# Performance work log

Measured on AMD Instinct MI355X. Metric: run time of the kernel, lower is better.

The kernel has to match this reference:

```python
import jax, jax.numpy as jnp
import numpy as np

B, T, F = 2, 128, 88          # batch, time frames, pitch bins (hard-coded 88)
HIDDEN = 64                    # LSTM input dim
N_UNIT = 64                    # channel dim (= 2 * lstm hidden 32)
N_HEAD = 4
HEAD_DIM = N_UNIT // N_HEAD    # 16
WINDOW = 7
N_LAYERS = 2
DIFF_STEPS = 100
LSTM_H = N_UNIT // 2           # 32 per direction


def setup_inputs() -> dict:
    key = jax.random.key(0)
    ks = jax.random.split(key, 12)
    s = 0.05
    inp = {
        'x': jax.random.normal(ks[0], (B, T * F, HIDDEN), jnp.float32),
        't': jax.random.randint(ks[1], (B,), 0, DIFF_STEPS, jnp.int32),
        # LSTM params, stacked [layer, direction, ...]; layer-1 input dim == 2*LSTM_H == HIDDEN
        'lstm_w_ih': s * jax.random.normal(ks[2], (N_LAYERS, 2, 4 * LSTM_H, HIDDEN), jnp.float32),
        'lstm_w_hh': s * jax.random.normal(ks[3], (N_LAYERS, 2, 4 * LSTM_H, LSTM_H), jnp.float32),
        'lstm_b_ih': s * jax.random.normal(ks[4], (N_LAYERS, 2, 4 * LSTM_H), jnp.float32),
        'lstm_b_hh': s * jax.random.normal(ks[5], (N_LAYERS, 2, 4 * LSTM_H), jnp.float32),
        # per-NA-layer params
        't_emb': s * jax.random.normal(ks[6], (N_LAYERS, DIFF_STEPS, N_UNIT), jnp.float32),
        'w_qkv': s * jax.random.normal(ks[7], (N_LAYERS, N_UNIT, 3 * N_UNIT), jnp.float32),
        'b_qkv': jnp.zeros((N_LAYERS, 3 * N_UNIT), jnp.float32),
        'rpb': s * jax.random.normal(ks[8], (N_LAYERS, N_HEAD, 2 * WINDOW - 1, 2 * WINDOW - 1), jnp.float32),
        'w_proj': s * jax.random.normal(ks[9], (N_LAYERS, N_UNIT, N_UNIT), jnp.float32),
        'b_proj': jnp.zeros((N_LAYERS, N_UNIT), jnp.float32),
    }
    return inp


def _lstm_dir(x, w_ih, w_hh, b_ih, b_hh, reverse):
    # x: [N, T, D]; pytorch gate order i, f, g, o
    N = x.shape[0]
    H = w_hh.shape[1]
    xs = jnp.swapaxes(x, 0, 1)
    if reverse:
        xs = xs[::-1]
    b = b_ih + b_hh
    def step(carry, xt):
        h, c = carry
        g = xt @ w_ih.T + h @ w_hh.T + b
        i, f, gg, o = jnp.split(g, 4, axis=-1)
        c = jax.nn.sigmoid(f) * c + jax.nn.sigmoid(i) * jnp.tanh(gg)
        h = jax.nn.sigmoid(o) * jnp.tanh(c)
        return (h, c), h
    h0 = jnp.zeros((N, H), x.dtype)
    _, hs = jax.lax.scan(step, (h0, h0), xs)
    if reverse:
        hs = hs[::-1]
    return jnp.swapaxes(hs, 0, 1)


def _bilstm(x, w_ih, w_hh, b_ih, b_hh):
    for l in range(w_ih.shape[0]):
        fwd = _lstm_dir(x, w_ih[l, 0], w_hh[l, 0], b_ih[l, 0], b_hh[l, 0], False)
        bwd = _lstm_dir(x, w_ih[l, 1], w_hh[l, 1], b_ih[l, 1], b_hh[l, 1], True)
        x = jnp.concatenate([fwd, bwd], axis=-1)
    return x


def _nbh(L, w):
    # NATTEN-style clamped (non-shrinking) neighborhood window per axis
    i = jnp.arange(L)
    start = jnp.clip(i - w // 2, 0, L - w)
    idx = start[:, None] + jnp.arange(w)[None, :]   # [L, w] absolute neighbor idx
    rel = idx - i[:, None] + (w - 1)                # [L, w] rel-pos-bias idx in [0, 2w-2]
    return idx, rel


def _na2d(x, t_idx, emb, wqkv, bqkv, rpb_l, wproj, bproj):
    # x: [B, Th, Tw, C]; diffusion-step conditioning via learned embedding add
    Bx, Th, Tw, C = x.shape
    h = x + emb[t_idx][:, None, None, :]
    qkv = (h @ wqkv + bqkv).reshape(Bx, Th, Tw, 3, N_HEAD, HEAD_DIM)
    q = jnp.moveaxis(qkv[..., 0, :, :], 3, 1) * (HEAD_DIM ** -0.5)  # [B,h,Th,Tw,d]
    k = jnp.moveaxis(qkv[..., 1, :, :], 3, 1)
    v = jnp.moveaxis(qkv[..., 2, :, :], 3, 1)
    ih, rh = _nbh(Th, WINDOW)
    iw, rw = _nbh(Tw, WINDOW)
    # gather windowed neighbors: [B,h,Th,Tw,w,w,d]
    kn = k[:, :, ih[:, None, :, None], iw[None, :, None, :], :]
    vn = v[:, :, ih[:, None, :, None], iw[None, :, None, :], :]
    bias = rpb_l[:, rh[:, None, :, None], rw[None, :, None, :]]     # [h,Th,Tw,w,w]
    logits = jnp.einsum('bhijd,bhijkld->bhijkl', q, kn) + bias[None]
    attn = jax.nn.softmax(logits.reshape(Bx, N_HEAD, Th, Tw, -1), axis=-1).reshape(logits.shape)
    out = jnp.einsum('bhijkl,bhijkld->bhijd', attn, vn)             # [B,h,Th,Tw,d]
    out = jnp.moveaxis(out, 1, 3).reshape(Bx, Th, Tw, C)
    return out @ wproj + bproj


def reference(x, t, lstm_w_ih, lstm_w_hh, lstm_b_ih, lstm_b_hh,
              t_emb, w_qkv, b_qkv, rpb, w_proj, b_proj):
    Bx = x.shape[0]
    Hin = x.shape[-1]
    Tt = x.shape[1] // F
    h = x.reshape(Bx, Tt, F, Hin).transpose(0, 2, 1, 3).reshape(Bx * F, Tt, Hin)
    h = _bilstm(h, lstm_w_ih, lstm_w_hh, lstm_b_ih, lstm_b_hh)      # [B*88, T, n_unit]
    # -> [B, T, 88, n_unit] 2D grid (height=T, width=88)
    h = h.reshape(Bx, F, Tt, N_UNIT).transpose(0, 2, 1, 3)
    for l in range(N_LAYERS):
        h = h + _na2d(h, t, t_emb[l], w_qkv[l], b_qkv[l], rpb[l], w_proj[l], b_proj[l])
    return h
```

## Files before the change

### kernel.cpp

```cpp
#include <hip/hip_runtime.h>
#include <math.h>

#define B_ 2
#define T_ 128
#define F_ 88
#define HID 64
#define NU 64
#define NH 4
#define HD 16
#define LH 32
#define NSEQ (B_*F_)
#define NTOK (B_*T_*F_)
#define NPOS (T_*F_)

__device__ __forceinline__ float fsig(float x) {
    return __builtin_amdgcn_rcpf(1.0f + __expf(-x));
}
__device__ __forceinline__ float ftanh(float x) {
    return 2.0f * __builtin_amdgcn_rcpf(1.0f + __expf(-2.0f*x)) - 1.0f;
}
__device__ __forceinline__ float rdlane(float v, int l) {
    return __uint_as_float(__builtin_amdgcn_readlane(__float_as_uint(v), l));
}

template<int LAYER>
__global__ void __launch_bounds__(256, 2) gg_kernel(
    const float* __restrict__ xin,
    const float* __restrict__ w_ih,
    const float* __restrict__ b_ih,
    const float* __restrict__ b_hh,
    float* __restrict__ G)
{
    __shared__ __align__(16) float xts[32][68];
    __shared__ __align__(16) float wsh[256][68];
    __shared__ float bsh[256];
    const int s  = blockIdx.x;
    const int t0 = blockIdx.y * 32;
    const int b = s / F_, f = s % F_;
    const int tid = threadIdx.x;

    for (int n = tid; n < 32*64; n += 256) {
        const int tt = n >> 6, k = n & 63;
        xts[tt][k] = (LAYER == 0)
            ? xin[(((size_t)b*T_ + t0+tt)*F_ + f)*HID + k]
            : xin[((size_t)s*T_ + t0+tt)*HID + k];
    }
    for (int n = tid; n < 256*64; n += 256) {
        const int row = n >> 6, k = n & 63;
        wsh[row][k] = w_ih[((size_t)LAYER*256 + row)*HID + k];
    }
    bsh[tid] = b_ih[LAYER*256 + tid] + b_hh[LAYER*256 + tid];
    __syncthreads();

    const int lane = tid & 63;
    const int g    = tid >> 6;
    const int dir  = g >> 1;
    const int th   = g & 1;
    const int rowA = dir*128 + lane;
    const int rowB = dir*128 + 64 + lane;

    float accA[16] = {}, accB[16] = {};
    #pragma unroll 4
    for (int k4 = 0; k4 < 16; k4++) {
        const float4 wA = *(const float4*)&wsh[rowA][k4*4];
        const float4 wB = *(const float4*)&wsh[rowB][k4*4];
        #pragma unroll
        for (int tt = 0; tt < 16; tt++) {
            const float4 xv = *(const float4*)&xts[th*16+tt][k4*4];
            accA[tt] += wA.x*xv.x + wA.y*xv.y + wA.z*xv.z + wA.w*xv.w;
            accB[tt] += wB.x*xv.x + wB.y*xv.y + wB.z*xv.z + wB.w*xv.w;
        }
    }
    const float bA = bsh[rowA], bB = bsh[rowB];
    float* gbase = G + (((size_t)(s*2+dir)*T_ + t0 + th*16)*LH + (lane & 31))*4
                     + (lane >> 5)*2;
    #pragma unroll
    for (int tt = 0; tt < 16; tt++) {
        float2 o; o.x = accA[tt] + bA; o.y = accB[tt] + bB;
        *(float2*)(gbase + (size_t)tt*128) = o;
    }
}

template<int LAYER>
__global__ void __launch_bounds__(64, 1) lstm_rec(
    const float* __restrict__ G,
    const float* __restrict__ w_hh,
    float* __restrict__ outp)
{
    __shared__ float hbuf[T_][LH];
    const int chain = blockIdx.x;
    const int s = chain >> 1, dir = chain & 1;
    const int b = s / F_, f = s % F_;
    const int lane = threadIdx.x;
    const int u = lane & 31;

    float wi[LH], wf[LH], wg[LH], wo[LH];
    {
        const float* wb = w_hh + (size_t)((LAYER*2+dir)*128)*LH;
        const float4* pi = (const float4*)(wb + (size_t)(0*LH + u)*LH);
        const float4* pf = (const float4*)(wb + (size_t)(1*LH + u)*LH);
        const float4* pg = (const float4*)(wb + (size_t)(2*LH + u)*LH);
        const float4* po = (const float4*)(wb + (size_t)(3*LH + u)*LH);
        #pragma unroll
        for (int k4 = 0; k4 < LH/4; k4++) {
            float4 a = pi[k4], bq = pf[k4], cq = pg[k4], dq = po[k4];
            wi[k4*4+0]=a.x;  wi[k4*4+1]=a.y;  wi[k4*4+2]=a.z;  wi[k4*4+3]=a.w;
            wf[k4*4+0]=bq.x; wf[k4*4+1]=bq.y; wf[k4*4+2]=bq.z; wf[k4*4+3]=bq.w;
            wg[k4*4+0]=cq.x; wg[k4*4+1]=cq.y; wg[k4*4+2]=cq.z; wg[k4*4+3]=cq.w;
            wo[k4*4+0]=dq.x; wo[k4*4+1]=dq.y; wo[k4*4+2]=dq.z; wo[k4*4+3]=dq.w;
        }
    }
    const float4* gp = (const float4*)G + (size_t)chain*T_*LH + u;
    #define GTIME(st) (dir ? (T_-1-(st)) : (st))

    float h = 0.f, c = 0.f;

    #define STEP(g4, stepi)                                                  \
    {                                                                        \
        float ci = (g4).x, cg = (g4).y, cf = (g4).z, co = (g4).w;            \
        float ci1 = 0.f, cg1 = 0.f, cf1 = 0.f, co1 = 0.f;                    \
        _Pragma("unroll")                                                    \
        for (int k = 0; k < 16; k++) {                                       \
            const float hk  = rdlane(h, k);                                  \
            const float hk2 = rdlane(h, k+16);                               \
            ci  += wi[k]*hk;     cg  += wg[k]*hk;                            \
            cf  += wf[k]*hk;     co  += wo[k]*hk;                            \
            ci1 += wi[k+16]*hk2; cg1 += wg[k+16]*hk2;                        \
            cf1 += wf[k+16]*hk2; co1 += wo[k+16]*hk2;                        \
        }                                                                    \
        const float ti = fsig(ci+ci1), tf = fsig(cf+cf1);                    \
        const float to = fsig(co+co1), tg = ftanh(cg+cg1);                   \
        c = tf*c + ti*tg;                                                    \
        h = to * ftanh(c);                                                   \
        if (lane < LH) hbuf[GTIME(stepi)][u] = h;                            \
    }

    float4 A[4], Bf[4];
    #pragma unroll
    for (int i = 0; i < 4; i++) A[i]  = gp[(size_t)GTIME(i)*LH];
    #pragma unroll
    for (int i = 0; i < 4; i++) Bf[i] = gp[(size_t)GTIME(4+i)*LH];

    #pragma unroll 1
    for (int grp = 0; grp < 32; grp++) {
        float4 P[4];
        const int pf4 = (grp < 30 ? grp + 2 : 31) * 4;
        #pragma unroll
        for (int i = 0; i < 4; i++) P[i] = gp[(size_t)GTIME(pf4+i)*LH];
        #pragma unroll
        for (int i = 0; i < 4; i++) { STEP(A[i], grp*4 + i); }
        #pragma unroll
        for (int i = 0; i < 4; i++) { A[i] = Bf[i]; Bf[i] = P[i]; }
    }
    #undef STEP
    #undef GTIME
    __syncthreads();

    const float4* l4 = (const float4*)&hbuf[0][0];
    if (LAYER == 0) {
        for (int idx = lane; idx < T_*8; idx += 64) {
            const int t = idx >> 3, q = idx & 7;
            *(float4*)&outp[((size_t)s*T_ + t)*NU + dir*LH + q*4] = l4[idx];
        }
    } else {
        for (int idx = lane; idx < T_*8; idx += 64) {
            const int t = idx >> 3, q = idx & 7;
            *(float4*)&outp[(((size_t)b*T_ + t)*F_ + f)*NU + dir*LH + q*4] = l4[idx];
        }
    }
}

__global__ void __launch_bounds__(256, 2) qkv_kernel(
    const float* __restrict__ hcur,
    const int*   __restrict__ tarr,
    const float* __restrict__ t_emb,
    const float* __restrict__ w_qkv,
    const float* __restrict__ b_qkv,
    const int layer,
    float* __restrict__ qb, float* __restrict__ kb, float* __restrict__ vb)
{
    __shared__ float as[64][65];
    __shared__ float wsh[64][64];
    const int m0 = blockIdx.x * 64;
    const int which = blockIdx.y;
    const int tid = threadIdx.x;
    const int bidx = m0 / NPOS;
    const int tb = tarr[bidx];
    const float* embp = t_emb + ((size_t)layer*100 + tb)*HID;

    for (int n = tid; n < 64*64; n += 256) {
        const int mm = n >> 6, k = n & 63;
        as[mm][k]  = hcur[((size_t)m0+mm)*64 + k] + embp[k];
        wsh[mm][k] = w_qkv[((size_t)layer*64 + mm)*192 + which*64 + k];
    }
    __syncthreads();

    const int tm = tid >> 4, tn = tid & 15;
    float acc[4][4] = {};
    for (int k = 0; k < 64; k++) {
        const float a0 = as[tm*4+0][k];
        const float a1 = as[tm*4+1][k];
        const float a2 = as[tm*4+2][k];
        const float a3 = as[tm*4+3][k];
        const float4 w = *(const float4*)&wsh[k][tn*4];
        acc[0][0]+=a0*w.x; acc[0][1]+=a0*w.y; acc[0][2]+=a0*w.z; acc[0][3]+=a0*w.w;
        acc[1][0]+=a1*w.x; acc[1][1]+=a1*w.y; acc[1][2]+=a1*w.z; acc[1][3]+=a1*w.w;
        acc[2][0]+=a2*w.x; acc[2][1]+=a2*w.y; acc[2][2]+=a2*w.z; acc[2][3]+=a2*w.w;
        acc[3][0]+=a3*w.x; acc[3][1]+=a3*w.y; acc[3][2]+=a3*w.z; acc[3][3]+=a3*w.w;
    }

    float* dst = (which == 0) ? qb : (which == 1) ? kb : vb;
    const float scale = (which == 0) ? 0.25f : 1.0f;
    const int hh = tn >> 2;
    const int dbase = (tn & 3) * 4;
    const float4 bv = *(const float4*)&b_qkv[(size_t)layer*192 + which*64 + tn*4];
    #pragma unroll
    for (int r = 0; r < 4; r++) {
        const int row = m0 + tm*4 + r;
        const int pos = row - bidx*NPOS;
        float4 o;
        o.x = (acc[r][0] + bv.x) * scale;
        o.y = (acc[r][1] + bv.y) * scale;
        o.z = (acc[r][2] + bv.z) * scale;
        o.w = (acc[r][3] + bv.w) * scale;
        *(float4*)&dst[(((size_t)bidx*NH + hh)*NPOS + pos)*HD + dbase] = o;
    }
}

__global__ void __launch_bounds__(192, 1) nattn_kernel(
    const float* __restrict__ qb,
    const float* __restrict__ kb,
    const float* __restrict__ vb,
    const float* __restrict__ rpb,
    const int layer,
    float* __restrict__ ao)
{
    __shared__ float ks[8][88][20];
    __shared__ float rp[169];
    const int blk = blockIdx.x;
    const int bh = blk & 7;
    const int it = blk >> 3;
    const int i0 = it*2;
    const int h  = bh & 3;
    const int bb = bh >> 2;
    const int tid = threadIdx.x;
    const int rs = min(max(i0-3, 0), T_-8);
    const float* kbase = kb + (size_t)bh*NPOS*HD;
    const float* vbase = vb + (size_t)bh*NPOS*HD;

    const bool act = (tid < 2*F_);
    const int isub = act ? (tid / F_) : 0;
    const int j    = act ? (tid - isub*F_) : 0;
    const int i    = i0 + isub;
    const int ihs  = min(max(i-3, 0), T_-7);
    const int ro   = ihs - rs;
    const int cw   = min(max(j-3, 0), F_-7);

    float4 q0, q1, q2, q3;
    if (act) {
        const float4* qp = (const float4*)&qb[((size_t)bh*NPOS + i*F_ + j)*HD];
        q0 = qp[0]; q1 = qp[1]; q2 = qp[2]; q3 = qp[3];
    }
    for (int n = tid; n < 169; n += 192)
        rp[n] = rpb[((size_t)layer*NH + h)*169 + n];
    for (int n4 = tid; n4 < 8*88*4; n4 += 192) {
        const int d4   = n4 & 3;
        const int rest = n4 >> 2;
        const int c    = rest % 88;
        const int r    = rest / 88;
        *(float4*)&ks[r][c][d4*4] =
            *(const float4*)&kbase[((size_t)(rs+r)*F_ + c)*HD + d4*4];
    }
    __syncthreads();

    float lg[49];
    if (act) {
        #pragma unroll
        for (int ki = 0; ki < 7; ki++) {
            const int rh = ihs + ki - i + 6;
            #pragma unroll
            for (int kj = 0; kj < 7; kj++) {
                const float4* kp = (const float4*)&ks[ro+ki][cw+kj][0];
                const float4 k0 = kp[0], k1 = kp[1], k2 = kp[2], k3 = kp[3];
                float d = q0.x*k0.x + q0.y*k0.y + q0.z*k0.z + q0.w*k0.w
                        + q1.x*k1.x + q1.y*k1.y + q1.z*k1.z + q1.w*k1.w
                        + q2.x*k2.x + q2.y*k2.y + q2.z*k2.z + q2.w*k2.w
                        + q3.x*k3.x + q3.y*k3.y + q3.z*k3.z + q3.w*k3.w;
                lg[ki*7+kj] = d + rp[rh*13 + (cw + kj - j + 6)];
            }
        }
        float m = lg[0];
        #pragma unroll
        for (int n = 1; n < 49; n++) m = fmaxf(m, lg[n]);
        float ssum = 0.f;
        #pragma unroll
        for (int n = 0; n < 49; n++) { lg[n] = __expf(lg[n] - m); ssum += lg[n]; }
        const float inv = __builtin_amdgcn_rcpf(ssum);
        #pragma unroll
        for (int n = 0; n < 49; n++) lg[n] *= inv;
    }
    __syncthreads();
    for (int n4 = tid; n4 < 8*88*4; n4 += 192) {
        const int d4   = n4 & 3;
        const int rest = n4 >> 2;
        const int c    = rest % 88;
        const int r    = rest / 88;
        *(float4*)&ks[r][c][d4*4] =
            *(const float4*)&vbase[((size_t)(rs+r)*F_ + c)*HD + d4*4];
    }
    __syncthreads();
    if (act) {
        float4 o0 = {0,0,0,0}, o1 = {0,0,0,0}, o2 = {0,0,0,0}, o3 = {0,0,0,0};
        #pragma unroll
        for (int ki = 0; ki < 7; ki++) {
            #pragma unroll
            for (int kj = 0; kj < 7; kj++) {
                const float a = lg[ki*7+kj];
                const float4* vp = (const float4*)&ks[ro+ki][cw+kj][0];
                const float4 v0 = vp[0], v1 = vp[1], v2 = vp[2], v3 = vp[3];
                o0.x += a*v0.x; o0.y += a*v0.y; o0.z += a*v0.z; o0.w += a*v0.w;
                o1.x += a*v1.x; o1.y += a*v1.y; o1.z += a*v1.z; o1.w += a*v1.w;
                o2.x += a*v2.x; o2.y += a*v2.y; o2.z += a*v2.z; o2.w += a*v2.w;
                o3.x += a*v3.x; o3.y += a*v3.y; o3.z += a*v3.z; o3.w += a*v3.w;
            }
        }
        float4* op = (float4*)&ao[(((size_t)bb*T_ + i)*F_ + j)*NU + h*HD];
        op[0]=o0; op[1]=o1; op[2]=o2; op[3]=o3;
    }
}

__global__ void __launch_bounds__(256, 2) proj_kernel(
    const float* __restrict__ ain,
    const float* __restrict__ hres,
    const float* __restrict__ w_proj,
    const float* __restrict__ b_proj,
    const int layer,
    float* __restrict__ outp)
{
    __shared__ float as[64][65];
    __shared__ float wsh[64][64];
    const int m0 = blockIdx.x * 64;
    const int tid = threadIdx.x;
    for (int n = tid; n < 64*64; n += 256) {
        const int mm = n >> 6, k = n & 63;
        as[mm][k]  = ain[((size_t)m0+mm)*64 + k];
        wsh[mm][k] = w_proj[(size_t)layer*4096 + n];
    }
    __syncthreads();
    const int tm = tid >> 4, tn = tid & 15;
    float acc[4][4] = {};
    for (int k = 0; k < 64; k++) {
        const float a0 = as[tm*4+0][k];
        const float a1 = as[tm*4+1][k];
        const float a2 = as[tm*4+2][k];
        const float a3 = as[tm*4+3][k];
        const float4 w = *(const float4*)&wsh[k][tn*4];
        acc[0][0]+=a0*w.x; acc[0][1]+=a0*w.y; acc[0][2]+=a0*w.z; acc[0][3]+=a0*w.w;
        acc[1][0]+=a1*w.x; acc[1][1]+=a1*w.y; acc[1][2]+=a1*w.z; acc[1][3]+=a1*w.w;
        acc[2][0]+=a2*w.x; acc[2][1]+=a2*w.y; acc[2][2]+=a2*w.z; acc[2][3]+=a2*w.w;
        acc[3][0]+=a3*w.x; acc[3][1]+=a3*w.y; acc[3][2]+=a3*w.z; acc[3][3]+=a3*w.w;
    }
    const float4 bv = *(const float4*)&b_proj[(size_t)layer*64 + tn*4];
    #pragma unroll
    for (int r = 0; r < 4; r++) {
        const int row = m0 + tm*4 + r;
        const float4 hv = *(const float4*)&hres[(size_t)row*64 + tn*4];
        float4 o;
        o.x = hv.x + acc[r][0] + bv.x;
        o.y = hv.y + acc[r][1] + bv.y;
        o.z = hv.z + acc[r][2] + bv.z;
        o.w = hv.w + acc[r][3] + bv.w;
        *(float4*)&outp[(size_t)row*64 + tn*4] = o;
    }
}

extern "C" void kernel_launch(void* const* d_in, const int* in_sizes, int n_in,
                              void* d_out, int out_size, void* d_ws, size_t ws_size,
                              hipStream_t stream) {
    const float* x      = (const float*)d_in[0];
    const int*   tarr   = (const int*)  d_in[1];
    const float* w_ih   = (const float*)d_in[2];
    const float* w_hh   = (const float*)d_in[3];
    const float* b_ih   = (const float*)d_in[4];
    const float* b_hh   = (const float*)d_in[5];
    const float* t_emb  = (const float*)d_in[6];
    const float* w_qkv  = (const float*)d_in[7];
    const float* b_qkv  = (const float*)d_in[8];
    const float* rpb    = (const float*)d_in[9];
    const float* w_proj = (const float*)d_in[10];
    const float* b_proj = (const float*)d_in[11];

    float* ws   = (float*)d_ws;
    const size_t CH = (size_t)NTOK * NU;
    float* hcur = ws;
    float* h0   = ws + CH;
    float* G    = ws + 2*CH;
    float* qbuf = ws + 2*CH;
    float* kbuf = ws + 3*CH;
    float* vbuf = ws + 4*CH;
    float* ao   = ws + 5*CH;
    float* outp = (float*)d_out;

    gg_kernel<0><<<dim3(NSEQ, T_/32), 256, 0, stream>>>(x,  w_ih, b_ih, b_hh, G);
    lstm_rec<0><<<NSEQ*2, 64, 0, stream>>>(G, w_hh, h0);
    gg_kernel<1><<<dim3(NSEQ, T_/32), 256, 0, stream>>>(h0, w_ih, b_ih, b_hh, G);
    lstm_rec<1><<<NSEQ*2, 64, 0, stream>>>(G, w_hh, hcur);

    for (int l = 0; l < 2; l++) {
        qkv_kernel<<<dim3(NTOK/64, 3), 256, 0, stream>>>(
            hcur, tarr, t_emb, w_qkv, b_qkv, l, qbuf, kbuf, vbuf);
        nattn_kernel<<<(T_/2)*8, 192, 0, stream>>>(
            qbuf, kbuf, vbuf, rpb, l, ao);
        proj_kernel<<<NTOK/64, 256, 0, stream>>>(
            ao, hcur, w_proj, b_proj, l, (l == 0) ? hcur : outp);
    }
}
```

Baseline: 285.1 us.

## Pack two LSTM chains per wavefront using half-wave shuffles

The recurrent LSTM kernel previously used a 64-lane wavefront for one 32-unit chain, so half the lanes duplicated work. It now assigns two sequences with the same direction to the two half-waves and launches half as many blocks. The hidden-state broadcast changes from scalar readlane to width-32 __shfl, which goes through ds_bpermute and costs more per step on the serial critical path. The trade is higher lane utilization and fewer blocks against slower per-step broadcasts.

```diff
diff --git a/kernel.cpp b/kernel.cpp
--- a/kernel.cpp
+++ b/kernel.cpp
@@ -18,9 +18,6 @@
 }
 __device__ __forceinline__ float ftanh(float x) {
     return 2.0f * __builtin_amdgcn_rcpf(1.0f + __expf(-2.0f*x)) - 1.0f;
-}
-__device__ __forceinline__ float rdlane(float v, int l) {
-    return __uint_as_float(__builtin_amdgcn_readlane(__float_as_uint(v), l));
 }
 
 template<int LAYER>
@@ -87,12 +84,16 @@
     const float* __restrict__ w_hh,
     float* __restrict__ outp)
 {
-    __shared__ float hbuf[T_][LH];
-    const int chain = blockIdx.x;
-    const int s = chain >> 1, dir = chain & 1;
+    __shared__ float hbuf[2][T_][LH];
+    const int p   = blockIdx.x;
+    const int dir = p & 1;
+    const int sA  = (p >> 1) * 2;
+    const int sB  = sA + 1;
+    const int lane = threadIdx.x;
+    const int u    = lane & 31;
+    const int half = lane >> 5;
+    const int s    = half ? sB : sA;
     const int b = s / F_, f = s % F_;
-    const int lane = threadIdx.x;
-    const int u = lane & 31;
 
     float wi[LH], wf[LH], wg[LH], wo[LH];
     {
@@ -110,6 +111,7 @@
             wo[k4*4+0]=dq.x; wo[k4*4+1]=dq.y; wo[k4*4+2]=dq.z; wo[k4*4+3]=dq.w;
         }
     }
+    const int chain = s*2 + dir;
     const float4* gp = (const float4*)G + (size_t)chain*T_*LH + u;
     #define GTIME(st) (dir ? (T_-1-(st)) : (st))
 
@@ -121,8 +123,8 @@
         float ci1 = 0.f, cg1 = 0.f, cf1 = 0.f, co1 = 0.f;                    \
         _Pragma("unroll")                                                    \
         for (int k = 0; k < 16; k++) {                                       \
-            const float hk  = rdlane(h, k);                                  \
-            const float hk2 = rdlane(h, k+16);                               \
+            const float hk  = __shfl(h, k, 32);          \
+            const float hk2 = __shfl(h, k+16, 32);                           \
             ci  += wi[k]*hk;     cg  += wg[k]*hk;                            \
             cf  += wf[k]*hk;     co  += wo[k]*hk;                            \
             ci1 += wi[k+16]*hk2; cg1 += wg[k+16]*hk2;                        \
@@ -132,7 +134,7 @@
         const float to = fsig(co+co1), tg = ftanh(cg+cg1);                   \
         c = tf*c + ti*tg;                                                    \
         h = to * ftanh(c);                                                   \
-        if (lane < LH) hbuf[GTIME(stepi)][u] = h;                            \
+        hbuf[half][GTIME(stepi)][u] = h;                                     \
     }
 
     float4 A[4], Bf[4];
@@ -156,14 +158,14 @@
     #undef GTIME
     __syncthreads();
 
-    const float4* l4 = (const float4*)&hbuf[0][0];
+    const float4* l4 = (const float4*)&hbuf[half][0][0];
     if (LAYER == 0) {
-        for (int idx = lane; idx < T_*8; idx += 64) {
+        for (int idx = u; idx < T_*8; idx += 32) {
             const int t = idx >> 3, q = idx & 7;
             *(float4*)&outp[((size_t)s*T_ + t)*NU + dir*LH + q*4] = l4[idx];
         }
     } else {
-        for (int idx = lane; idx < T_*8; idx += 64) {
+        for (int idx = u; idx < T_*8; idx += 32) {
             const int t = idx >> 3, q = idx & 7;
             *(float4*)&outp[(((size_t)b*T_ + t)*F_ + f)*NU + dir*LH + q*4] = l4[idx];
         }
@@ -402,9 +404,9 @@
     float* outp = (float*)d_out;
 
     gg_kernel<0><<<dim3(NSEQ, T_/32), 256, 0, stream>>>(x,  w_ih, b_ih, b_hh, G);
-    lstm_rec<0><<<NSEQ*2, 64, 0, stream>>>(G, w_hh, h0);
+    lstm_rec<0><<<NSEQ, 64, 0, stream>>>(G, w_hh, h0);
     gg_kernel<1><<<dim3(NSEQ, T_/32), 256, 0, stream>>>(h0, w_ih, b_ih, b_hh, G);
-    lstm_rec<1><<<NSEQ*2, 64, 0, stream>>>(G, w_hh, hcur);
+    lstm_rec<1><<<NSEQ, 64, 0, stream>>>(G, w_hh, hcur);
 
     for (int l = 0; l < 2; l++) {
         qkv_kernel<<<dim3(NTOK/64, 3), 256, 0, stream>>>(
```

Result: faster. 277.8 us (-2.6%).
